# Kernel tuning notes

Measured on AMD Instinct MI355X. Metric: run time of the kernel, lower is better.

The kernel has to match this reference:

```python
import jax, jax.numpy as jnp
import numpy as np


def setup_inputs() -> dict:
    key = jax.random.key(0)
    ks = jax.random.split(key, 12)
    B, S, D, Q = 16, 2048, 1024, 64
    std = 1.0 / np.sqrt(D)
    return {
        "raw": jax.random.normal(ks[0], (B, S, D), jnp.float32),
        "post_dec": jax.random.normal(ks[1], (B, S, D), jnp.float32),
        "mask": jnp.ones((B, S), dtype=bool),
        "questions": jax.random.uniform(ks[2], (Q, D), jnp.float32),
        "Wk": jax.random.normal(ks[3], (D, D), jnp.float32) * std,
        "bk": jnp.zeros((D,), jnp.float32),
        "Wi": jax.random.normal(ks[4], (1, D), jnp.float32) * std,
        "bi": jnp.zeros((1,), jnp.float32),
        "Wo": jax.random.normal(ks[5], (D, D), jnp.float32) * std,
        "bo": jnp.zeros((D,), jnp.float32),
        "Wu1": jax.random.normal(ks[6], (1, D), jnp.float32) * std,
        "bu1": jnp.zeros((1,), jnp.float32),
        "Wu2": jax.random.normal(ks[7], (1, D), jnp.float32) * std,
        "bu2": jnp.zeros((1,), jnp.float32),
        "b1": jax.random.uniform(ks[8], (1,), jnp.float32),
    }


def reference(raw, post_dec, mask, questions, Wk, bk, Wi, bi, Wo, bo, Wu1, bu1, Wu2, bu2, b1):
    D = raw.shape[-1]
    Q = questions.shape[0]
    inv_sqrt_d = jnp.float32(1.0 / np.sqrt(D))
    inv_sqrt_q = jnp.float32(1.0 / np.sqrt(Q))

    # ---- create_A_matrix: write external memory A [Q, D] ----
    k = raw @ Wk.T + bk                                   # [B,S,D]
    v = raw * jax.nn.sigmoid(raw @ Wi.T + bi)             # ignore gate, [B,S,D]
    scores = jnp.einsum('qd,bsd->bqs', questions, k) * inv_sqrt_d  # [B,Q,S]
    scores = jnp.where(mask[:, None, :], scores, jnp.float32(-1e9))
    attn = jax.nn.softmax(scores, axis=-1)
    A = jnp.einsum('bqs,bsd->qd', attn, v) / jnp.float32(raw.shape[0])  # mean over batch

    # ---- get_data_from_A_matrix: read memory ----
    ko = post_dec @ Wo.T + bo                              # [B,S,D]
    s2 = jnp.einsum('bsd,qd->bsq', ko, questions) * inv_sqrt_q  # [B,S,Q]
    A2 = jax.nn.softmax(s2, axis=-1) @ A                   # [B,S,D]
    gate = jax.nn.sigmoid((post_dec @ Wu1.T + bu1) + (A2 @ Wu2.T + bu2) + b1)  # [B,S,1]
    return post_dec + A2 * gate
```

## Files before the change

kernel.cpp:

```cpp
#include <hip/hip_runtime.h>
#include <math.h>

#define NBATCH 16
#define SEQ    2048
#define BS     32768
#define DIM    1024
#define NQ     64
#define CKS    68
#define INV_SQRT_D 0.03125f
#define INV_SQRT_Q 0.125f

#define OFF_QT   0
#define OFF_CKT  65536
#define OFF_COT  135168
#define OFF_S1   204800
#define OFF_G2   2334720
#define OFF_A    2367488
#define OFF_BO   2433024
#define OFF_AW   2433088
#define OFF_CKP  2433152
#define OFF_COP  2474112
#define OFF_W2B  2515072
#define OFF_AMT  3563648

typedef short bf16x8 __attribute__((ext_vector_type(8)));
typedef float f32x4 __attribute__((ext_vector_type(4)));

union V8 { uint4 u4; bf16x8 s8; uint32_t u[4]; };

__device__ __forceinline__ f32x4 mfma16(bf16x8 a, bf16x8 b, f32x4 c) {
  return __builtin_amdgcn_mfma_f32_16x16x32_bf16(a, b, c, 0, 0, 0);
}
__device__ __forceinline__ uint32_t f2b(float f) { return __float_as_uint(f); }
__device__ __forceinline__ uint32_t packtr(float lo, float hi) {
  return __builtin_amdgcn_perm(f2b(hi), f2b(lo), 0x07060302u);
}
__device__ __forceinline__ uint32_t rne1(float f) {
  uint32_t u = f2b(f);
  return (u + 0x7FFFu + ((u >> 16) & 1u)) >> 16;
}
__device__ __forceinline__ uint32_t packrne(float lo, float hi) {
  return rne1(lo) | (rne1(hi) << 16);
}
__device__ __forceinline__ bf16x8 ldg8(const unsigned short* p) {
  V8 v; v.u4 = *(const uint4*)p; return v.s8;
}
__device__ __forceinline__ bf16x8 pack8(const float* p) {
  float4 a = *(const float4*)(p);
  float4 b = *(const float4*)(p + 4);
  V8 v;
  v.u[0] = packtr(a.x, a.y);
  v.u[1] = packtr(a.z, a.w);
  v.u[2] = packtr(b.x, b.y);
  v.u[3] = packtr(b.z, b.w);
  return v.s8;
}

__device__ __forceinline__ void pipe_load(const float* pd, const unsigned short* mb, int k0,
                                          float4& pa, float4& pb, uint4* c) {
  pa = *(const float4*)(pd + k0);
  pb = *(const float4*)(pd + k0 + 4);
#pragma unroll
  for (int mt = 0; mt < 5; ++mt)
    c[mt] = *(const uint4*)(mb + (size_t)mt*16*DIM + k0);
}
__device__ __forceinline__ void pipe_comp(const float4& pa, const float4& pb, const uint4* c,
                                          f32x4* acc) {
  V8 v;
  v.u[0] = packtr(pa.x, pa.y);
  v.u[1] = packtr(pa.z, pa.w);
  v.u[2] = packtr(pb.x, pb.y);
  v.u[3] = packtr(pb.z, pb.w);
  bf16x8 b = v.s8;
#pragma unroll
  for (int mt = 0; mt < 5; ++mt) {
    V8 a; a.u4 = c[mt];
    acc[mt] = mfma16(a.s8, b, acc[mt]);
  }
}

__global__ __launch_bounds__(256) void kpre(const float* __restrict__ questions,
                                            const float* __restrict__ bo,
                                            const float* __restrict__ Wi,
                                            const float* __restrict__ Wu1,
                                            float* __restrict__ ws) {
  __shared__ float red[4];
  float* qT    = ws + OFF_QT;
  float* CKT   = ws + OFF_CKT;
  float* COT   = ws + OFF_COT;
  float* biasO = ws + OFF_BO;
  int bid = blockIdx.x, tid = threadIdx.x;
  if (bid < 64) {
    int q = bid;
    float acc = 0.f;
    for (int e = tid; e < DIM; e += 256) {
      float v = questions[q*DIM + e];
      qT[e*NQ + q] = v;
      acc += v * bo[e];
    }
    for (int off = 32; off > 0; off >>= 1) acc += __shfl_xor(acc, off, 64);
    if ((tid & 63) == 0) red[tid >> 6] = acc;
    __syncthreads();
    if (tid == 0) biasO[q] = red[0] + red[1] + red[2] + red[3];
  } else {
    int r = bid - 64;
    int h = r & 1;
    const float* src = (r < 2) ? Wi : Wu1;
    float* dst = (r < 2) ? CKT : COT;
    int d = h*512 + tid;
    dst[d*CKS + 64] = src[d];
    d += 256;
    dst[d*CKS + 64] = src[d];
  }
}

__global__ __launch_bounds__(256) void k0_proj(const float* __restrict__ Wk,
                                               const float* __restrict__ Wo,
                                               float* __restrict__ ws) {
  const float* qT = ws + OFF_QT;
  int bid = blockIdx.x;
  int mat = bid & 1;
  int kc  = (bid >> 1) & 3;
  int dt  = bid >> 3;
  const float* W = mat ? Wo : Wk;
  float* dest = ws + (mat ? OFF_COT : OFF_CKT);
  int d0 = dt * 64, e0 = kc * 256;
  __shared__ __align__(16) float aL[32*CKS];
  __shared__ __align__(16) float bL[32*CKS];
  int tid = threadIdx.x;
  int tx = tid & 15, ty = tid >> 4;
  float acc[4][4] = {};
  for (int ek = e0; ek < e0 + 256; ek += 32) {
    for (int idx = tid; idx < 32*64; idx += 256) {
      int kk = idx >> 6, j = idx & 63;
      aL[kk*CKS + j] = qT[(ek + kk)*NQ + j];
      bL[kk*CKS + j] = W[(size_t)(ek + kk)*DIM + d0 + j];
    }
    __syncthreads();
#pragma unroll
    for (int kk = 0; kk < 32; kk++) {
      float4 av = *(const float4*)&aL[kk*CKS + ty*4];
      float4 bv = *(const float4*)&bL[kk*CKS + tx*4];
      float a[4] = {av.x, av.y, av.z, av.w};
      float b[4] = {bv.x, bv.y, bv.z, bv.w};
#pragma unroll
      for (int r = 0; r < 4; ++r)
#pragma unroll
        for (int c = 0; c < 4; ++c)
          acc[r][c] += a[r] * b[c];
    }
    __syncthreads();
  }
#pragma unroll
  for (int r = 0; r < 4; ++r)
#pragma unroll
    for (int c = 0; c < 4; ++c)
      atomicAdd(&dest[(d0 + tx*4 + c)*CKS + ty*4 + r], acc[r][c]);
}

__global__ __launch_bounds__(256) void kpack(float* __restrict__ ws) {
  int bid = blockIdx.x;
  int row = bid % 80;
  int mat = bid / 80;
  const float* src = ws + (mat ? OFF_COT : OFF_CKT);
  unsigned short* dst = (unsigned short*)(ws + (mat ? OFF_COP : OFF_CKP));
  int d = threadIdx.x * 4;
  float v[4];
#pragma unroll
  for (int i = 0; i < 4; ++i)
    v[i] = (row <= 64) ? src[(d + i)*CKS + row] : 0.f;
  uint2 o;
  o.x = packrne(v[0], v[1]);
  o.y = packrne(v[2], v[3]);
  *(uint2*)(dst + (size_t)row*DIM + d) = o;
}

__global__ __launch_bounds__(256, 2) void k1_scores(const float* __restrict__ raw,
                                                    float* __restrict__ ws) {
  const unsigned short* CKp = (const unsigned short*)(ws + OFF_CKP);
  float* S1 = ws + OFF_S1;
  int tid = threadIdx.x;
  int wave = tid >> 6, lane = tid & 63, lm = lane & 15, quad = lane >> 4;
  int tb = blockIdx.x*64 + wave*16;
  const float* pd = raw + (size_t)(tb + lm)*DIM + quad*8;
  const unsigned short* mb = CKp + (size_t)lm*DIM + quad*8;
  f32x4 acc[5] = {};
  float4 pfa[4], pfb[4];
  uint4  pco[4][5];
#pragma unroll
  for (int s = 0; s < 4; ++s) pipe_load(pd, mb, s*32, pfa[s], pfb[s], pco[s]);
  for (int k0 = 0; k0 < DIM - 128; k0 += 128) {
#pragma unroll
    for (int s = 0; s < 4; ++s) {
      pipe_comp(pfa[s], pfb[s], pco[s], acc);
      pipe_load(pd, mb, k0 + 128 + s*32, pfa[s], pfb[s], pco[s]);
    }
  }
#pragma unroll
  for (int s = 0; s < 4; ++s) pipe_comp(pfa[s], pfb[s], pco[s], acc);
#pragma unroll
  for (int mt = 0; mt < 4; ++mt)
#pragma unroll
    for (int reg = 0; reg < 4; ++reg)
      S1[(size_t)(mt*16 + quad*4 + reg)*BS + tb + lm] = acc[mt][reg];
  if (quad == 0)
    S1[(size_t)64*BS + tb + lm] = acc[4][0];
}

__global__ __launch_bounds__(256) void k2_softmax(const float* __restrict__ biP,
                                                  float* __restrict__ ws) {
  const float* S1 = ws + OFF_S1;
  uint32_t* w2u = (uint32_t*)(ws + OFF_W2B);
  __shared__ float redA[4];
  __shared__ float redB[4];
  int bid = blockIdx.x;
  int q = bid & 63, b = bid >> 6;
  int tid = threadIdx.x, wave = tid >> 6, lane = tid & 63;
  const float* row = S1 + (size_t)q*BS + b*SEQ + tid*8;
  float4 xa = *(const float4*)row;
  float4 xb = *(const float4*)(row + 4);
  const float* isc = S1 + (size_t)64*BS + b*SEQ + tid*8;
  float4 ia = *(const float4*)isc;
  float4 ib = *(const float4*)(isc + 4);
  float x[8] = {xa.x, xa.y, xa.z, xa.w, xb.x, xb.y, xb.z, xb.w};
  float is[8] = {ia.x, ia.y, ia.z, ia.w, ib.x, ib.y, ib.z, ib.w};
#pragma unroll
  for (int i = 0; i < 8; ++i) x[i] *= INV_SQRT_D;
  float m = -1e30f;
#pragma unroll
  for (int i = 0; i < 8; ++i) m = fmaxf(m, x[i]);
  for (int off = 32; off > 0; off >>= 1) m = fmaxf(m, __shfl_xor(m, off, 64));
  if (lane == 0) redA[wave] = m;
  __syncthreads();
  m = fmaxf(fmaxf(redA[0], redA[1]), fmaxf(redA[2], redA[3]));
  float e[8];
  float s = 0.f;
#pragma unroll
  for (int i = 0; i < 8; ++i) { e[i] = __expf(x[i] - m); s += e[i]; }
  for (int off = 32; off > 0; off >>= 1) s += __shfl_xor(s, off, 64);
  if (lane == 0) redB[wave] = s;
  __syncthreads();
  s = redB[0] + redB[1] + redB[2] + redB[3];
  float inv = 1.f / s;
  float bi0 = biP[0];
  float w[8];
#pragma unroll
  for (int i = 0; i < 8; ++i) {
    float g = (1.f / (1.f + __expf(-(is[i] + bi0)))) * (1.f / (float)NBATCH);
    w[i] = e[i] * inv * g;
  }
  uint4 o;
  o.x = packtr(w[0], w[1]);
  o.y = packtr(w[2], w[3]);
  o.z = packtr(w[4], w[5]);
  o.w = packtr(w[6], w[7]);
  *(uint4*)&w2u[((size_t)q*BS + b*SEQ + tid*8) >> 1] = o;
}

#define K3STR 36
__global__ __launch_bounds__(256) void k3_accA(const float* __restrict__ raw,
                                               float* __restrict__ ws) {
  const unsigned short* w2b = (const unsigned short*)(ws + OFF_W2B);
  float* A = ws + OFF_A;
  int bid = blockIdx.x;
  int dt = bid & 7, tc = bid >> 3;
  int d0 = dt*128;
  int tid = threadIdx.x;
  int wave = tid >> 6, lane = tid & 63, lm = lane & 15, quad = lane >> 4;
  int pq = tid & 7;
  int dr = tid >> 3;
  __shared__ __align__(16) uint32_t ldsB[128*K3STR];
  f32x4 acc[4][2] = {};
  for (int tk = tc*1024; tk < tc*1024 + 1024; tk += 64) {
    float4 rv[8];
#pragma unroll
    for (int r = 0; r < 8; ++r)
      rv[r] = *(const float4*)&raw[(size_t)(tk + pq*8 + r)*DIM + d0 + dr*4];
    __syncthreads();
    int pc = ((pq ^ (dr & 7)) << 2);
#pragma unroll
    for (int j = 0; j < 4; ++j) {
      const float* f0 = (const float*)&rv[0];
      uint4 wv;
      wv.x = packtr(((const float*)&rv[0])[j], ((const float*)&rv[1])[j]);
      wv.y = packtr(((const float*)&rv[2])[j], ((const float*)&rv[3])[j]);
      wv.z = packtr(((const float*)&rv[4])[j], ((const float*)&rv[5])[j]);
      wv.w = packtr(((const float*)&rv[6])[j], ((const float*)&rv[7])[j]);
      (void)f0;
      *(uint4*)&ldsB[(dr*4 + j)*K3STR + pc] = wv;
    }
    __syncthreads();
#pragma unroll
    for (int ks = 0; ks < 2; ++ks) {
      bf16x8 af[4];
#pragma unroll
      for (int mt = 0; mt < 4; ++mt)
        af[mt] = ldg8(w2b + (size_t)(mt*16 + lm)*BS + tk + ks*32 + quad*8);
      bf16x8 bfr[2];
#pragma unroll
      for (int nt = 0; nt < 2; ++nt) {
        int rowd = wave*32 + nt*16 + lm;
        int pcr = (((ks*4 + quad) ^ ((rowd >> 2) & 7)) << 2);
        V8 v; v.u4 = *(const uint4*)&ldsB[rowd*K3STR + pcr];
        bfr[nt] = v.s8;
      }
#pragma unroll
      for (int mt = 0; mt < 4; ++mt)
#pragma unroll
        for (int nt = 0; nt < 2; ++nt)
          acc[mt][nt] = mfma16(af[mt], bfr[nt], acc[mt][nt]);
    }
  }
#pragma unroll
  for (int mt = 0; mt < 4; ++mt)
#pragma unroll
    for (int nt = 0; nt < 2; ++nt)
#pragma unroll
      for (int reg = 0; reg < 4; ++reg)
        atomicAdd(&A[(mt*16 + quad*4 + reg)*DIM + d0 + wave*32 + nt*16 + lm],
                  acc[mt][nt][reg]);
}

__global__ __launch_bounds__(256) void k3b_aw(const float* __restrict__ Wu2,
                                              float* __restrict__ ws) {
  const float* A = ws + OFF_A;
  float* aw = ws + OFF_AW;
  unsigned short* at = (unsigned short*)(ws + OFF_AMT);
  __shared__ float red[4];
  int q = blockIdx.x, tid = threadIdx.x;
  float acc = 0.f;
  for (int d = tid; d < DIM; d += 256) {
    float v = A[q*DIM + d];
    acc += v * Wu2[d];
    at[(size_t)d*NQ + q] = (unsigned short)rne1(v);
  }
  for (int off = 32; off > 0; off >>= 1) acc += __shfl_xor(acc, off, 64);
  if ((tid & 63) == 0) red[tid >> 6] = acc;
  __syncthreads();
  if (tid == 0) aw[q] = red[0] + red[1] + red[2] + red[3];
}

#define T4S  67
#define W4SU 36
__global__ __launch_bounds__(256, 2) void k4_phase2(const float* __restrict__ post_dec,
                                                    const float* __restrict__ bu1p,
                                                    const float* __restrict__ bu2p,
                                                    const float* __restrict__ b1p,
                                                    float* __restrict__ out,
                                                    float* __restrict__ ws) {
  const unsigned short* COp = (const unsigned short*)(ws + OFF_COP);
  const unsigned short* AmT = (const unsigned short*)(ws + OFF_AMT);
  const float* biasO = ws + OFF_BO;
  const float* aw    = ws + OFF_AW;
  __shared__ __align__(16) float    Tall[4][16*T4S];
  __shared__ __align__(16) uint32_t wAll[4][16*W4SU];
  __shared__ float gAll[4][16];
  int tid = threadIdx.x;
  int wave = tid >> 6, lane = tid & 63, lm = lane & 15, quad = lane >> 4;
  int t0 = blockIdx.x*64 + wave*16;

  const float* pd = post_dec + (size_t)(t0 + lm)*DIM + quad*8;
  const unsigned short* mb = COp + (size_t)lm*DIM + quad*8;
  f32x4 acc[5] = {};
  {
    float4 pfa[4], pfb[4];
    uint4  pco[4][5];
#pragma unroll
    for (int s = 0; s < 4; ++s) pipe_load(pd, mb, s*32, pfa[s], pfb[s], pco[s]);
    for (int k0 = 0; k0 < DIM - 128; k0 += 128) {
#pragma unroll
      for (int s = 0; s < 4; ++s) {
        pipe_comp(pfa[s], pfb[s], pco[s], acc);
        pipe_load(pd, mb, k0 + 128 + s*32, pfa[s], pfb[s], pco[s]);
      }
    }
#pragma unroll
    for (int s = 0; s < 4; ++s) pipe_comp(pfa[s], pfb[s], pco[s], acc);
  }
  float* Tw = Tall[wave];
#pragma unroll
  for (int mt = 0; mt < 4; ++mt)
#pragma unroll
    for (int reg = 0; reg < 4; ++reg)
      Tw[lm*T4S + mt*16 + quad*4 + reg] = acc[mt][reg];
  if (quad == 0) Tw[lm*T4S + 64] = acc[4][0];

  {
    int r = lane >> 2, h = lane & 3;
    float x[16];
#pragma unroll
    for (int i = 0; i < 16; ++i)
      x[i] = (Tw[r*T4S + h*16 + i] + biasO[h*16 + i]) * INV_SQRT_Q;
    float m = x[0];
#pragma unroll
    for (int i = 1; i < 16; ++i) m = fmaxf(m, x[i]);
    m = fmaxf(m, __shfl_xor(m, 1, 64));
    m = fmaxf(m, __shfl_xor(m, 2, 64));
    float e[16], s = 0.f, sa = 0.f;
#pragma unroll
    for (int i = 0; i < 16; ++i) {
      e[i] = __expf(x[i] - m);
      s += e[i];
      sa += e[i] * aw[h*16 + i];
    }
    s  += __shfl_xor(s, 1, 64);  s  += __shfl_xor(s, 2, 64);
    sa += __shfl_xor(sa, 1, 64); sa += __shfl_xor(sa, 2, 64);
    float inv = 1.f / s;
    uint32_t* wr = wAll[wave] + r*W4SU + h*8;
#pragma unroll
    for (int i2 = 0; i2 < 8; ++i2)
      wr[i2] = packtr(e[2*i2]*inv, e[2*i2+1]*inv);
    if (h == 0) {
      float garg = Tw[r*T4S + 64] + bu1p[0] + sa*inv + bu2p[0] + b1p[0];
      gAll[wave][r] = 1.f / (1.f + __expf(-garg));
    }
  }

  const unsigned short* wS = (const unsigned short*)wAll[wave];
  bf16x8 am[2];
#pragma unroll
  for (int ks = 0; ks < 2; ++ks) {
    V8 v; v.u4 = *(const uint4*)&wS[lm*(W4SU*2) + ks*32 + quad*8];
    am[ks] = v.s8;
  }
  float gv[4];
#pragma unroll
  for (int reg = 0; reg < 4; ++reg) gv[reg] = gAll[wave][quad*4 + reg];

  const float* prs = post_dec + (size_t)(t0 + quad*4)*DIM + lm;
  float*       pot = out      + (size_t)(t0 + quad*4)*DIM + lm;
  const unsigned short* amtb = AmT + (size_t)lm*NQ + quad*8;

  uint4 bA[8], bB[8];
  float rA[16], rB[16];
  auto c_load = [&](int d0, uint4* bb, float* rr) {
#pragma unroll
    for (int ks = 0; ks < 2; ++ks)
#pragma unroll
      for (int nt = 0; nt < 4; ++nt)
        bb[ks*4 + nt] = *(const uint4*)(amtb + (size_t)(d0 + nt*16)*NQ + ks*32);
#pragma unroll
    for (int reg = 0; reg < 4; ++reg)
#pragma unroll
      for (int nt = 0; nt < 4; ++nt)
        rr[reg*4 + nt] = prs[(size_t)reg*DIM + d0 + nt*16];
  };
  auto c_comp = [&](int d0, const uint4* bb, const float* rr) {
    f32x4 acc2[4] = {};
#pragma unroll
    for (int ks = 0; ks < 2; ++ks)
#pragma unroll
      for (int nt = 0; nt < 4; ++nt) {
        V8 v; v.u4 = bb[ks*4 + nt];
        acc2[nt] = mfma16(am[ks], v.s8, acc2[nt]);
      }
#pragma unroll
    for (int nt = 0; nt < 4; ++nt)
#pragma unroll
      for (int reg = 0; reg < 4; ++reg)
        pot[(size_t)reg*DIM + d0 + nt*16] = rr[reg*4 + nt] + acc2[nt][reg] * gv[reg];
  };

  c_load(0, bA, rA);
#pragma unroll
  for (int d0 = 0; d0 < DIM; d0 += 128) {
    if (d0 + 64 < DIM)  c_load(d0 + 64, bB, rB);
    c_comp(d0, bA, rA);
    if (d0 + 128 < DIM) c_load(d0 + 128, bA, rA);
    c_comp(d0 + 64, bB, rB);
  }
}

extern "C" void kernel_launch(void* const* d_in, const int* in_sizes, int n_in,
                              void* d_out, int out_size, void* d_ws, size_t ws_size,
                              hipStream_t stream) {
  const float* raw       = (const float*)d_in[0];
  const float* post_dec  = (const float*)d_in[1];
  const float* questions = (const float*)d_in[3];
  const float* Wk        = (const float*)d_in[4];
  const float* Wi        = (const float*)d_in[6];
  const float* bi        = (const float*)d_in[7];
  const float* Wo        = (const float*)d_in[8];
  const float* bo        = (const float*)d_in[9];
  const float* Wu1       = (const float*)d_in[10];
  const float* bu1       = (const float*)d_in[11];
  const float* Wu2       = (const float*)d_in[12];
  const float* bu2       = (const float*)d_in[13];
  const float* b1        = (const float*)d_in[14];
  float* out = (float*)d_out;
  float* ws  = (float*)d_ws;

  hipMemsetAsync(ws + OFF_CKT, 0, (size_t)2*DIM*CKS*sizeof(float), stream);
  hipMemsetAsync(ws + OFF_A,   0, (size_t)NQ*DIM*sizeof(float), stream);

  kpre<<<68, 256, 0, stream>>>(questions, bo, Wi, Wu1, ws);
  k0_proj<<<128, 256, 0, stream>>>(Wk, Wo, ws);
  kpack<<<160, 256, 0, stream>>>(ws);
  k1_scores<<<512, 256, 0, stream>>>(raw, ws);
  k2_softmax<<<1024, 256, 0, stream>>>(bi, ws);
  k3_accA<<<256, 256, 0, stream>>>(raw, ws);
  k3b_aw<<<64, 256, 0, stream>>>(Wu2, ws);
  k4_phase2<<<512, 256, 0, stream>>>(post_dec, bu1, bu2, b1, out, ws);
}
```

Measured before the change: 557.0 us.

## Stage projection GEMM tiles via global_load_lds double buffering; split accA over more blocks

The register-prefetch pipelines in k1_scores and k4_phase2 are replaced with a double-buffered LDS staging scheme. It uses global_load_lds 16-byte direct loads with XOR-swizzled layouts, so each block loads its 64-row activation tile and the 80-row packed weight tile into shared memory once and all waves share them. This is meant to remove redundant per-wave weight loads and cut register pressure. k3_accA also halves its token range per block and doubles its grid to raise parallelism. The cost is extra LDS use (about 36KB per block) and a barrier per chunk, and launch_bounds minimum-occupancy hints are dropped.

```diff
diff --git a/kernel.cpp b/kernel.cpp
--- a/kernel.cpp
+++ b/kernel.cpp
@@ -14,7 +14,6 @@
 #define OFF_CKT  65536
 #define OFF_COT  135168
 #define OFF_S1   204800
-#define OFF_G2   2334720
 #define OFF_A    2367488
 #define OFF_BO   2433024
 #define OFF_AW   2433088
@@ -55,27 +54,57 @@
   v.u[3] = packtr(b.z, b.w);
   return v.s8;
 }
-
-__device__ __forceinline__ void pipe_load(const float* pd, const unsigned short* mb, int k0,
-                                          float4& pa, float4& pb, uint4* c) {
-  pa = *(const float4*)(pd + k0);
-  pb = *(const float4*)(pd + k0 + 4);
-#pragma unroll
-  for (int mt = 0; mt < 5; ++mt)
-    c[mt] = *(const uint4*)(mb + (size_t)mt*16*DIM + k0);
-}
-__device__ __forceinline__ void pipe_comp(const float4& pa, const float4& pb, const uint4* c,
-                                          f32x4* acc) {
-  V8 v;
-  v.u[0] = packtr(pa.x, pa.y);
-  v.u[1] = packtr(pa.z, pa.w);
-  v.u[2] = packtr(pb.x, pb.y);
-  v.u[3] = packtr(pb.z, pb.w);
-  bf16x8 b = v.s8;
-#pragma unroll
-  for (int mt = 0; mt < 5; ++mt) {
-    V8 a; a.u4 = c[mt];
-    acc[mt] = mfma16(a.s8, b, acc[mt]);
+__device__ __forceinline__ void gll16(const void* g, void* lds) {
+  __builtin_amdgcn_global_load_lds(
+      (const __attribute__((address_space(1))) unsigned int*)g,
+      (__attribute__((address_space(3))) unsigned int*)lds, 16, 0, 0);
+}
+
+__device__ __forceinline__ void stage_chunk(const float* __restrict__ srcPD,
+                                            const unsigned short* __restrict__ srcCO,
+                                            float* pdl, unsigned short* col,
+                                            int t0, int k0, int wave, int lane) {
+  int quad = lane >> 4, lm = lane & 15;
+#pragma unroll
+  for (int j = 0; j < 4; ++j) {
+    int t = (wave*4 + j)*4 + quad;
+    const float* src = srcPD + (size_t)(t0 + t)*DIM + k0 + ((lm ^ (t & 7)) << 2);
+    gll16(src, (char*)pdl + (size_t)(wave*4 + j)*1024);
+  }
+  int r8 = lane >> 3, g8 = lane & 7;
+#pragma unroll
+  for (int j = 0; j < 3; ++j) {
+    int i = j*4 + wave;
+    if (i < 10) {
+      int r = i*8 + r8;
+      const unsigned short* src = srcCO + (size_t)r*DIM + k0 + ((g8 ^ (r & 7)) << 3);
+      gll16(src, (char*)col + (size_t)i*1024);
+    }
+  }
+}
+__device__ __forceinline__ void comp_chunk(const float* pdl, const unsigned short* col,
+                                           int wave, int lane, f32x4* acc) {
+  int quad = lane >> 4, lm = lane & 15;
+  int tl = wave*16 + lm;
+  const float* prow = pdl + tl*64;
+#pragma unroll
+  for (int ks = 0; ks < 2; ++ks) {
+    int p0 = (ks*8 + quad*2)     ^ (lm & 7);
+    int p1 = (ks*8 + quad*2 + 1) ^ (lm & 7);
+    float4 b0 = *(const float4*)(prow + p0*4);
+    float4 b1 = *(const float4*)(prow + p1*4);
+    V8 v;
+    v.u[0] = packtr(b0.x, b0.y);
+    v.u[1] = packtr(b0.z, b0.w);
+    v.u[2] = packtr(b1.x, b1.y);
+    v.u[3] = packtr(b1.z, b1.w);
+#pragma unroll
+    for (int mt = 0; mt < 5; ++mt) {
+      int r = mt*16 + lm;
+      int g = (ks*4 + quad) ^ (lm & 7);
+      V8 a; a.u4 = *(const uint4*)(col + r*64 + g*8);
+      acc[mt] = mfma16(a.s8, v.s8, acc[mt]);
+    }
   }
 }
 
@@ -175,29 +204,25 @@
   *(uint2*)(dst + (size_t)row*DIM + d) = o;
 }
 
-__global__ __launch_bounds__(256, 2) void k1_scores(const float* __restrict__ raw,
-                                                    float* __restrict__ ws) {
+__global__ __launch_bounds__(256) void k1_scores(const float* __restrict__ raw,
+                                                 float* __restrict__ ws) {
   const unsigned short* CKp = (const unsigned short*)(ws + OFF_CKP);
   float* S1 = ws + OFF_S1;
+  __shared__ __align__(16) float          PDL[2][64*64];
+  __shared__ __align__(16) unsigned short COL[2][80*64];
   int tid = threadIdx.x;
   int wave = tid >> 6, lane = tid & 63, lm = lane & 15, quad = lane >> 4;
-  int tb = blockIdx.x*64 + wave*16;
-  const float* pd = raw + (size_t)(tb + lm)*DIM + quad*8;
-  const unsigned short* mb = CKp + (size_t)lm*DIM + quad*8;
+  int t0 = blockIdx.x*64;
   f32x4 acc[5] = {};
-  float4 pfa[4], pfb[4];
-  uint4  pco[4][5];
-#pragma unroll
-  for (int s = 0; s < 4; ++s) pipe_load(pd, mb, s*32, pfa[s], pfb[s], pco[s]);
-  for (int k0 = 0; k0 < DIM - 128; k0 += 128) {
-#pragma unroll
-    for (int s = 0; s < 4; ++s) {
-      pipe_comp(pfa[s], pfb[s], pco[s], acc);
-      pipe_load(pd, mb, k0 + 128 + s*32, pfa[s], pfb[s], pco[s]);
-    }
-  }
-#pragma unroll
-  for (int s = 0; s < 4; ++s) pipe_comp(pfa[s], pfb[s], pco[s], acc);
+  stage_chunk(raw, CKp, PDL[0], COL[0], t0, 0, wave, lane);
+  __syncthreads();
+  for (int c = 0; c < 16; ++c) {
+    if (c + 1 < 16)
+      stage_chunk(raw, CKp, PDL[(c+1)&1], COL[(c+1)&1], t0, (c+1)*64, wave, lane);
+    comp_chunk(PDL[c&1], COL[c&1], wave, lane, acc);
+    __syncthreads();
+  }
+  int tb = t0 + wave*16;
 #pragma unroll
   for (int mt = 0; mt < 4; ++mt)
 #pragma unroll
@@ -271,7 +296,7 @@
   int dr = tid >> 3;
   __shared__ __align__(16) uint32_t ldsB[128*K3STR];
   f32x4 acc[4][2] = {};
-  for (int tk = tc*1024; tk < tc*1024 + 1024; tk += 64) {
+  for (int tk = tc*512; tk < tc*512 + 512; tk += 64) {
     float4 rv[8];
 #pragma unroll
     for (int r = 0; r < 8; ++r)
@@ -342,40 +367,34 @@
 
 #define T4S  67
 #define W4SU 36
-__global__ __launch_bounds__(256, 2) void k4_phase2(const float* __restrict__ post_dec,
-                                                    const float* __restrict__ bu1p,
-                                                    const float* __restrict__ bu2p,
-                                                    const float* __restrict__ b1p,
-                                                    float* __restrict__ out,
-                                                    float* __restrict__ ws) {
+__global__ __launch_bounds__(256) void k4_phase2(const float* __restrict__ post_dec,
+                                                 const float* __restrict__ bu1p,
+                                                 const float* __restrict__ bu2p,
+                                                 const float* __restrict__ b1p,
+                                                 float* __restrict__ out,
+                                                 float* __restrict__ ws) {
   const unsigned short* COp = (const unsigned short*)(ws + OFF_COP);
   const unsigned short* AmT = (const unsigned short*)(ws + OFF_AMT);
   const float* biasO = ws + OFF_BO;
   const float* aw    = ws + OFF_AW;
+  __shared__ __align__(16) float          PDL[2][64*64];
+  __shared__ __align__(16) unsigned short COL[2][80*64];
   __shared__ __align__(16) float    Tall[4][16*T4S];
   __shared__ __align__(16) uint32_t wAll[4][16*W4SU];
   __shared__ float gAll[4][16];
   int tid = threadIdx.x;
   int wave = tid >> 6, lane = tid & 63, lm = lane & 15, quad = lane >> 4;
-  int t0 = blockIdx.x*64 + wave*16;
-
-  const float* pd = post_dec + (size_t)(t0 + lm)*DIM + quad*8;
-  const unsigned short* mb = COp + (size_t)lm*DIM + quad*8;
+  int t0 = blockIdx.x*64;
+  int tw0 = t0 + wave*16;
+
   f32x4 acc[5] = {};
-  {
-    float4 pfa[4], pfb[4];
-    uint4  pco[4][5];
-#pragma unroll
-    for (int s = 0; s < 4; ++s) pipe_load(pd, mb, s*32, pfa[s], pfb[s], pco[s]);
-    for (int k0 = 0; k0 < DIM - 128; k0 += 128) {
-#pragma unroll
-      for (int s = 0; s < 4; ++s) {
-        pipe_comp(pfa[s], pfb[s], pco[s], acc);
-        pipe_load(pd, mb, k0 + 128 + s*32, pfa[s], pfb[s], pco[s]);
-      }
-    }
-#pragma unroll
-    for (int s = 0; s < 4; ++s) pipe_comp(pfa[s], pfb[s], pco[s], acc);
+  stage_chunk(post_dec, COp, PDL[0], COL[0], t0, 0, wave, lane);
+  __syncthreads();
+  for (int c = 0; c < 16; ++c) {
+    if (c + 1 < 16)
+      stage_chunk(post_dec, COp, PDL[(c+1)&1], COL[(c+1)&1], t0, (c+1)*64, wave, lane);
+    comp_chunk(PDL[c&1], COL[c&1], wave, lane, acc);
+    __syncthreads();
   }
   float* Tw = Tall[wave];
 #pragma unroll
@@ -427,8 +446,8 @@
 #pragma unroll
   for (int reg = 0; reg < 4; ++reg) gv[reg] = gAll[wave][quad*4 + reg];
 
-  const float* prs = post_dec + (size_t)(t0 + quad*4)*DIM + lm;
-  float*       pot = out      + (size_t)(t0 + quad*4)*DIM + lm;
+  const float* prs = post_dec + (size_t)(tw0 + quad*4)*DIM + lm;
+  float*       pot = out      + (size_t)(tw0 + quad*4)*DIM + lm;
   const unsigned short* amtb = AmT + (size_t)lm*NQ + quad*8;
 
   uint4 bA[8], bB[8];
@@ -498,7 +517,7 @@
   kpack<<<160, 256, 0, stream>>>(ws);
   k1_scores<<<512, 256, 0, stream>>>(raw, ws);
   k2_softmax<<<1024, 256, 0, stream>>>(bi, ws);
-  k3_accA<<<256, 256, 0, stream>>>(raw, ws);
+  k3_accA<<<512, 256, 0, stream>>>(raw, ws);
   k3b_aw<<<64, 256, 0, stream>>>(Wu2, ws);
   k4_phase2<<<512, 256, 0, stream>>>(post_dec, bu1, bu2, b1, out, ws);
 }
```

Result: faster. 530.9 us (-4.7%).
